# Kernel tuning notes

Measured on AMD Instinct MI355X. Metric: run time of the kernel, lower is better.

Reference implementation:

```python
import jax, jax.numpy as jnp
import numpy as np
import math

IN_DIM = 256
OUT_DIM = 256
H = 4
DK = OUT_DIM // H  # 64
N = 40000
E = 300000
T = 2  # node types
R = 3  # relations: 0:(A->B), 1:(B->A), 2:(A->B)


def setup_inputs() -> dict:
    key = jax.random.key(0)
    ks = jax.random.split(key, 24)
    def xavier(k, shape):
        fan_in, fan_out = shape[-2], shape[-1]
        lim = math.sqrt(6.0 / (fan_in + fan_out))
        return jax.random.uniform(k, shape, jnp.float32, -lim, lim)
    inp = {
        "hA": jax.random.normal(ks[0], (N, IN_DIM), jnp.float32),
        "hB": jax.random.normal(ks[1], (N, IN_DIM), jnp.float32),
        "src0": jax.random.randint(ks[2], (E,), 0, N, jnp.int32),
        "dst0": jax.random.randint(ks[3], (E,), 0, N, jnp.int32),
        "src1": jax.random.randint(ks[4], (E,), 0, N, jnp.int32),
        "dst1": jax.random.randint(ks[5], (E,), 0, N, jnp.int32),
        "src2": jax.random.randint(ks[6], (E,), 0, N, jnp.int32),
        "dst2": jax.random.randint(ks[7], (E,), 0, N, jnp.int32),
        # per-node-type linear weights, stacked [T, in, out]
        "Wk": xavier(ks[8], (T, IN_DIM, OUT_DIM)),
        "bk": jnp.zeros((T, OUT_DIM), jnp.float32),
        "Wq": xavier(ks[9], (T, IN_DIM, OUT_DIM)),
        "bq": jnp.zeros((T, OUT_DIM), jnp.float32),
        "Wv": xavier(ks[10], (T, IN_DIM, OUT_DIM)),
        "bv": jnp.zeros((T, OUT_DIM), jnp.float32),
        "Wa": xavier(ks[11], (T, OUT_DIM, OUT_DIM)),
        "ba": jnp.zeros((T, OUT_DIM), jnp.float32),
        "rel_att": xavier(ks[12], (R, H, DK, DK)),
        "rel_msg": xavier(ks[13], (R, H, DK, DK)),
        "rel_pri": jnp.ones((R, H), jnp.float32),
        "skip": jnp.ones((T,), jnp.float32),
    }
    return inp


def _hgt_forward(hA, hB, Wk, bk, Wq, bq, Wv, bv, Wa, ba,
                 rel_att, rel_msg, rel_pri, skip, edges):
    h = [hA, hB]
    sqrt_dk = math.sqrt(DK)

    def proj(W, b, x, t):
        return (x @ W[t] + b[t]).reshape(-1, H, DK)

    def rel_agg(r, s, d, src, dst):
        # relation-specific transforms
        k = jnp.einsum('nhi,hij->nhj', proj(Wk, bk, h[s], s), rel_att[r])
        v = jnp.einsum('nhi,hij->nhj', proj(Wv, bv, h[s], s), rel_msg[r])
        q = proj(Wq, bq, h[d], d)
        nd = h[d].shape[0]
        # per-edge dot-product attention score [E, H]
        score = jnp.einsum('ehd,ehd->eh', q[dst], k[src]) * rel_pri[r] / sqrt_dk
        # edge softmax normalized by destination node
        m = jax.ops.segment_max(score, dst, num_segments=nd)
        e = jnp.exp(score - m[dst])
        denom = jax.ops.segment_sum(e, dst, num_segments=nd)
        attn = e / denom[dst]
        # weighted scatter-sum aggregation -> [nd, H, DK]
        return jax.ops.segment_sum(v[src] * attn[:, :, None], dst, num_segments=nd)

    (src0, dst0), (src1, dst1), (src2, dst2) = edges
    agg0 = rel_agg(0, 0, 1, src0, dst0)  # A -> B
    agg1 = rel_agg(1, 1, 0, src1, dst1)  # B -> A
    agg2 = rel_agg(2, 0, 1, src2, dst2)  # A -> B

    # cross_reducer='mean' over etypes per destination type
    t_A = agg1.reshape(-1, OUT_DIM)
    t_B = ((agg0 + agg2) * 0.5).reshape(-1, OUT_DIM)

    def ts_aggr(t, n_id, h_dst):
        alpha = jax.nn.sigmoid(skip[n_id])
        trans = t @ Wa[n_id] + ba[n_id]  # dropout p=0.0 -> identity
        return trans * alpha + h_dst * (1.0 - alpha)

    out_A = ts_aggr(t_A, 0, hA)
    out_B = ts_aggr(t_B, 1, hB)
    return jnp.stack([out_A, out_B])  # [2, N, OUT_DIM]


def reference(hA, hB, src0, dst0, src1, dst1, src2, dst2,
              Wk, bk, Wq, bq, Wv, bv, Wa, ba,
              rel_att, rel_msg, rel_pri, skip):
    edges = ((src0, dst0), (src1, dst1), (src2, dst2))
    return _hgt_forward(hA, hB, Wk, bk, Wq, bq, Wv, bv, Wa, ba,
                        rel_att, rel_msg, rel_pri, skip, edges)
```

## Files before the change

kernel.cpp:

```cpp
#include <hip/hip_runtime.h>

#define NN 40000
#define EE 300000
#define DIM 256
#define NHD 4
#define CAP 64
#define LOG2E 1.4426950408889634f

typedef __attribute__((ext_vector_type(8))) short bfrag;
typedef __attribute__((ext_vector_type(4))) float fx4;

static __device__ __forceinline__ float bflo(unsigned u) {
  union { unsigned i; float f; } v; v.i = u << 16; return v.f;
}
static __device__ __forceinline__ float bfhi(unsigned u) {
  union { unsigned i; float f; } v; v.i = u & 0xffff0000u; return v.f;
}
static __device__ __forceinline__ unsigned short f2bf(float f) {
  union { float f; unsigned i; } v; v.f = f;
  unsigned x = v.i;
  return (unsigned short)((x + 0x7fffu + ((x >> 16) & 1u)) >> 16);
}
static __device__ __forceinline__ void gload_lds16(const unsigned short* g, unsigned short* l) {
  __builtin_amdgcn_global_load_lds((const __attribute__((address_space(1))) void*)g,
                                   (__attribute__((address_space(3))) void*)l, 16, 0, 0);
}

static __device__ __forceinline__ void map_rc(int L, int NC, int NR, int& rb, int& cb) {
  int per = 8 * NC;
  int g = L / per;
  int base = g * 8;
  int rig = NR - base; if (rig > 8) rig = 8;
  int idx = L - g * per;
  rb = base + idx % rig;
  cb = idx / rig;
}

static __device__ __forceinline__ void gemm_core64(const unsigned short* __restrict__ X,
                                                   const unsigned short* __restrict__ WT,
                                                   int R0, int C0,
                                                   fx4 acc[2][4],
                                                   unsigned short* ldsA,
                                                   unsigned short* ldsB) {
  const int tid = threadIdx.x;
  const int wave = tid >> 6, lane = tid & 63;
  const int li = lane & 15, lk = lane >> 4;
  const int wr = wave >> 1, wc = wave & 1;
  const int lr = lane >> 3;
  const int swz = ((lane & 7) ^ lr) * 8;
#pragma unroll
  for (int kt = 0; kt < 4; ++kt) {
    const int k0 = kt * 64;
    if (kt) __syncthreads();
#pragma unroll
    for (int i = 0; i < 6; ++i) {
      int g = wave * 6 + i;
      if (g < 8) gload_lds16(X + (size_t)(R0 + g * 8 + lr) * DIM + k0 + swz, ldsA + g * 512);
      else       gload_lds16(WT + (size_t)(C0 + (g - 8) * 8 + lr) * DIM + k0 + swz, ldsB + (g - 8) * 512);
    }
    __syncthreads();
#pragma unroll
    for (int ks = 0; ks < 2; ++ks) {
      bfrag a[2], b[4];
      const int chb = (lk + ks * 4) ^ (li & 7);
#pragma unroll
      for (int mt = 0; mt < 2; ++mt)
        a[mt] = *(const bfrag*)(ldsA + (wr * 32 + mt * 16 + li) * 64 + chb * 8);
#pragma unroll
      for (int nt = 0; nt < 4; ++nt)
        b[nt] = *(const bfrag*)(ldsB + (wc * 64 + nt * 16 + li) * 64 + chb * 8);
#pragma unroll
      for (int mt = 0; mt < 2; ++mt)
#pragma unroll
        for (int nt = 0; nt < 4; ++nt)
          acc[mt][nt] = __builtin_amdgcn_mfma_f32_16x16x32_bf16(a[mt], b[nt], acc[mt][nt], 0, 0, 0);
    }
  }
}

__global__ __launch_bounds__(256) void prep_all(
    const float* __restrict__ hA, const float* __restrict__ hB,
    unsigned short* __restrict__ XA, unsigned short* __restrict__ XB,
    const float* __restrict__ Wk, const float* __restrict__ bk,
    const float* __restrict__ Wq, const float* __restrict__ bq,
    const float* __restrict__ Wv, const float* __restrict__ bv,
    const float* __restrict__ Wa,
    const float* __restrict__ rel_att, const float* __restrict__ rel_msg,
    const float* __restrict__ rel_pri,
    unsigned short* __restrict__ WT_A, unsigned short* __restrict__ WT_B,
    unsigned short* __restrict__ WaT, float* __restrict__ biasA, float* __restrict__ biasB,
    const int* __restrict__ src0, const int* __restrict__ dst0,
    const int* __restrict__ src1, const int* __restrict__ dst1,
    const int* __restrict__ src2, const int* __restrict__ dst2,
    int* __restrict__ cnt, int* __restrict__ bkt) {
  if (blockIdx.x >= 6084) {
    long id = (long)(blockIdx.x - 6084) * 256 + threadIdx.x;
    const long half = (long)NN * DIM / 8;
    const float4* src; unsigned short* dst; long o;
    if (id < half) { src = (const float4*)hA; dst = XA; o = id; }
    else           { src = (const float4*)hB; dst = XB; o = id - half; }
    float4 a = src[o * 2], b = src[o * 2 + 1];
    uint4 pk;
    pk.x = (unsigned)f2bf(a.x) | ((unsigned)f2bf(a.y) << 16);
    pk.y = (unsigned)f2bf(a.z) | ((unsigned)f2bf(a.w) << 16);
    pk.z = (unsigned)f2bf(b.x) | ((unsigned)f2bf(b.y) << 16);
    pk.w = (unsigned)f2bf(b.z) | ((unsigned)f2bf(b.w) << 16);
    ((uint4*)dst)[o] = pk;
    return;
  }
  if (blockIdx.x >= 2568) {
    int bb = blockIdx.x - 2568;
    int r = bb / 1172;
    int e = (bb % 1172) * 256 + threadIdx.x;
    if (e >= EE) return;
    const int* src = r == 0 ? src0 : (r == 1 ? src1 : src2);
    const int* dst = r == 0 ? dst0 : (r == 1 ? dst1 : dst2);
    int d = dst[e];
    int pos = atomicAdd(&cnt[r * NN + d], 1);
    if (pos < CAP) bkt[(size_t)r * NN * CAP + d * CAP + pos] = src[e];
    return;
  }
  int id = blockIdx.x * 256 + threadIdx.x;
  if (id < 262144) {
    int c = id >> 8, i = id & 255;
    int br = c >> 9, w = c & 511, h = w >> 7, ww = w & 127;
    int iskv = (ww >> 2) & 1;
    int j = (ww >> 3) * 4 + (ww & 3);
    int r = br ? 2 : 0;
    const float* W  = iskv ? Wv : Wk;
    const float* RM = iskv ? rel_msg : rel_att;
    const float* wrow = W + i * 256 + h * 64;
    const float* rm = RM + (size_t)((r * NHD + h) * 64) * 64 + j;
    float s = 0.f;
#pragma unroll 8
    for (int l = 0; l < 64; l++) s += wrow[l] * rm[l * 64];
    if (!iskv) s *= rel_pri[r * NHD + h] * 0.125f * LOG2E;
    WT_A[c * 256 + i] = f2bf(s);
    return;
  }
  id -= 262144;
  if (id < 65536) {
    int c = id >> 8, i = id & 255;
    WT_A[(1024 + c) * 256 + i] = f2bf(Wq[i * 256 + c]);
    return;
  }
  id -= 65536;
  if (id < 131072) {
    int c = id >> 8, i = id & 255;
    int h = c >> 7, ww = c & 127;
    int iskv = (ww >> 2) & 1;
    int j = (ww >> 3) * 4 + (ww & 3);
    const float* W  = iskv ? Wv : Wk;
    const float* RM = iskv ? rel_msg : rel_att;
    const float* wrow = W + 65536 + i * 256 + h * 64;
    const float* rm = RM + (size_t)((1 * NHD + h) * 64) * 64 + j;
    float s = 0.f;
#pragma unroll 8
    for (int l = 0; l < 64; l++) s += wrow[l] * rm[l * 64];
    if (!iskv) s *= rel_pri[1 * NHD + h] * 0.125f * LOG2E;
    WT_B[c * 256 + i] = f2bf(s);
    return;
  }
  id -= 131072;
  if (id < 65536) {
    int c = id >> 8, i = id & 255;
    WT_B[(512 + c) * 256 + i] = f2bf(Wq[65536 + i * 256 + c]);
    return;
  }
  id -= 65536;
  if (id < 131072) {
    int t = id >> 16, rem = id & 65535, c = rem >> 8, i = rem & 255;
    WaT[t * 65536 + c * 256 + i] = f2bf(Wa[t * 65536 + i * 256 + c]);
    return;
  }
  id -= 131072;
  if (id < 2048) {
    if (id < 1280) {
      int c = id; float s;
      if (c < 1024) {
        int br = c >> 9, w = c & 511, h = w >> 7, ww = w & 127;
        int iskv = (ww >> 2) & 1;
        int j = (ww >> 3) * 4 + (ww & 3);
        int r = br ? 2 : 0;
        const float* B  = iskv ? bv : bk;
        const float* RM = iskv ? rel_msg : rel_att;
        s = 0.f;
        for (int l = 0; l < 64; l++)
          s += B[h * 64 + l] * RM[(size_t)((r * NHD + h) * 64 + l) * 64 + j];
        if (!iskv) s *= rel_pri[r * NHD + h] * 0.125f * LOG2E;
      } else s = bq[c - 1024];
      biasA[c] = s;
    } else {
      int c = id - 1280; float s;
      if (c < 512) {
        int h = c >> 7, ww = c & 127;
        int iskv = (ww >> 2) & 1;
        int j = (ww >> 3) * 4 + (ww & 3);
        const float* B  = iskv ? bv : bk;
        const float* RM = iskv ? rel_msg : rel_att;
        s = 0.f;
        for (int l = 0; l < 64; l++)
          s += B[256 + h * 64 + l] * RM[(size_t)((1 * NHD + h) * 64 + l) * 64 + j];
        if (!iskv) s *= rel_pri[1 * NHD + h] * 0.125f * LOG2E;
      } else s = bq[256 + (c - 512)];
      biasB[c] = s;
    }
  }
}

__global__ __launch_bounds__(256) void gemm_kvq(const unsigned short* __restrict__ XA,
                                                const unsigned short* __restrict__ XB,
                                                const unsigned short* __restrict__ WT_A,
                                                const unsigned short* __restrict__ WT_B,
                                                const float* __restrict__ biasA,
                                                const float* __restrict__ biasB,
                                                unsigned short* __restrict__ OutA,
                                                unsigned short* __restrict__ OutB) {
  __shared__ unsigned short ldsA[4096], ldsB[8192];
  const unsigned short* X; const unsigned short* WT; const float* bias;
  unsigned short* Out; int ldOut, NC, Lb;
  if (blockIdx.x < 6250) { X = XA; WT = WT_A; bias = biasA; Out = OutA; ldOut = 1280; NC = 10; Lb = blockIdx.x; }
  else                   { X = XB; WT = WT_B; bias = biasB; Out = OutB; ldOut = 768;  NC = 6;  Lb = blockIdx.x - 6250; }
  fx4 acc[2][4] = {};
  int rb, cb; map_rc(Lb, NC, 625, rb, cb);
  const int R0 = rb * 64, C0 = cb * 128;
  gemm_core64(X, WT, R0, C0, acc, ldsA, ldsB);
  const int wave = threadIdx.x >> 6, lane = threadIdx.x & 63;
  const int li = lane & 15, lk = lane >> 4;
  const int wr = wave >> 1, wc = wave & 1;
#pragma unroll
  for (int mt = 0; mt < 2; mt++)
#pragma unroll
    for (int nt = 0; nt < 4; nt++) {
      int col = C0 + wc * 64 + nt * 16 + li;
      float bcol = bias[col];
      int rbase = R0 + wr * 32 + mt * 16 + lk * 4;
#pragma unroll
      for (int i = 0; i < 4; i++)
        Out[(long)(rbase + i) * ldOut + col] = f2bf(acc[mt][nt][i] + bcol);
    }
}

template<int LD>
static __device__ __forceinline__ void proc_bucket(const unsigned short* __restrict__ Out,
                                                   int c, int srcs, int kvoff,
                                                   float q0, float q1, float q2, float q3,
                                                   float& L, float& A0, float& A1, float& A2, float& A3) {
  const uint4 Z = {0u, 0u, 0u, 0u};
  auto ldx = [&](int E) -> uint4 {
    int s = __builtin_amdgcn_readlane(srcs, E & 63);
    return *(const uint4*)(Out + (size_t)s * LD + kvoff);
  };
  auto proc = [&](uint4 u) {
    float pp = q0 * bflo(u.x) + q1 * bfhi(u.x) + q2 * bflo(u.y) + q3 * bfhi(u.y);
    pp += __shfl_xor(pp, 1); pp += __shfl_xor(pp, 2);
    pp += __shfl_xor(pp, 4); pp += __shfl_xor(pp, 8);
    float p = exp2f(pp);
    L += p;
    A0 += p * bflo(u.z); A1 += p * bfhi(u.z);
    A2 += p * bflo(u.w); A3 += p * bfhi(u.w);
  };
  uint4 e0 = Z, e1 = Z, e2 = Z, e3 = Z;
  if (0 < c) e0 = ldx(0);
  if (1 < c) e1 = ldx(1);
  if (2 < c) e2 = ldx(2);
  if (3 < c) e3 = ldx(3);
  for (int e = 0; e < c; e += 4) {
    uint4 f0 = Z, f1 = Z, f2 = Z, f3 = Z;
    if (e + 4 < c) f0 = ldx(e + 4);
    if (e + 5 < c) f1 = ldx(e + 5);
    if (e + 6 < c) f2 = ldx(e + 6);
    if (e + 7 < c) f3 = ldx(e + 7);
    proc(e0);
    if (e + 1 < c) proc(e1);
    if (e + 2 < c) proc(e2);
    if (e + 3 < c) proc(e3);
    e0 = f0; e1 = f1; e2 = f2; e3 = f3;
  }
}

__global__ __launch_bounds__(256) void agg_all(const unsigned short* __restrict__ OutA,
                                               const unsigned short* __restrict__ OutB,
                                               const int* __restrict__ cnt,
                                               const int* __restrict__ bkt,
                                               unsigned short* __restrict__ tA,
                                               unsigned short* __restrict__ tB) {
  int wid = (blockIdx.x * 256 + threadIdx.x) >> 6;
  int lane = threadIdx.x & 63;
  int h = lane >> 4, li = lane & 15;
  int qoff = h * 64 + li * 4;
  int kvoff = h * 128 + li * 8;
  if (wid < NN) {
    int n = wid;
    uint2 qr = *(const uint2*)(OutB + (size_t)n * 768 + 512 + qoff);
    float q0 = bflo(qr.x), q1 = bfhi(qr.x), q2 = bflo(qr.y), q3 = bfhi(qr.y);
    int c0 = min(cnt[n], CAP);
    int c2 = min(cnt[2 * NN + n], CAP);
    int s0 = (lane < c0) ? bkt[(size_t)n * CAP + lane] : 0;
    int s2 = (lane < c2) ? bkt[(size_t)2 * NN * CAP + n * CAP + lane] : 0;
    float l0 = 0.f, b00 = 0.f, b01 = 0.f, b02 = 0.f, b03 = 0.f;
    float l2 = 0.f, b20 = 0.f, b21 = 0.f, b22 = 0.f, b23 = 0.f;
    proc_bucket<1280>(OutA,       c0, s0, kvoff, q0, q1, q2, q3, l0, b00, b01, b02, b03);
    proc_bucket<1280>(OutA + 512, c2, s2, kvoff, q0, q1, q2, q3, l2, b20, b21, b22, b23);
    float i0 = (l0 > 0.f) ? 0.5f / l0 : 0.f;
    float i2 = (l2 > 0.f) ? 0.5f / l2 : 0.f;
    float r0 = b00 * i0 + b20 * i2, r1 = b01 * i0 + b21 * i2;
    float r2 = b02 * i0 + b22 * i2, r3 = b03 * i0 + b23 * i2;
    uint2 pk;
    pk.x = (unsigned)f2bf(r0) | ((unsigned)f2bf(r1) << 16);
    pk.y = (unsigned)f2bf(r2) | ((unsigned)f2bf(r3) << 16);
    *(uint2*)(tB + (size_t)n * DIM + qoff) = pk;
  } else if (wid < 2 * NN) {
    int n = wid - NN;
    uint2 qr = *(const uint2*)(OutA + (size_t)n * 1280 + 1024 + qoff);
    float q0 = bflo(qr.x), q1 = bfhi(qr.x), q2 = bflo(qr.y), q3 = bfhi(qr.y);
    int c = min(cnt[NN + n], CAP);
    int s1 = (lane < c) ? bkt[(size_t)NN * CAP + n * CAP + lane] : 0;
    float l = 0.f, a0 = 0.f, a1 = 0.f, a2 = 0.f, a3 = 0.f;
    proc_bucket<768>(OutB, c, s1, kvoff, q0, q1, q2, q3, l, a0, a1, a2, a3);
    float inv = (l > 0.f) ? 1.f / l : 0.f;
    uint2 pk;
    pk.x = (unsigned)f2bf(a0 * inv) | ((unsigned)f2bf(a1 * inv) << 16);
    pk.y = (unsigned)f2bf(a2 * inv) | ((unsigned)f2bf(a3 * inv) << 16);
    *(uint2*)(tA + (size_t)n * DIM + qoff) = pk;
  }
}

__global__ __launch_bounds__(256) void gemm_final2(const unsigned short* __restrict__ tA,
                                                   const unsigned short* __restrict__ tB,
                                                   const unsigned short* __restrict__ XA,
                                                   const unsigned short* __restrict__ XB,
                                                   const unsigned short* __restrict__ WaT,
                                                   const float* __restrict__ ba,
                                                   const float* __restrict__ skip,
                                                   float* __restrict__ outp) {
  __shared__ unsigned short ldsA[4096], ldsB[8192];
  const int t = blockIdx.y;
  const unsigned short* Tt = t ? tB : tA;
  const unsigned short* hin = t ? XB : XA;
  float* op = outp + (size_t)t * NN * DIM;
  fx4 acc[2][4] = {};
  int rb, cb; map_rc(blockIdx.x, 2, 625, rb, cb);
  const int R0 = rb * 64, C0 = cb * 128;
  gemm_core64(Tt, WaT + t * 65536, R0, C0, acc, ldsA, ldsB);
  const int wave = threadIdx.x >> 6, lane = threadIdx.x & 63;
  const int li = lane & 15, lk = lane >> 4;
  const int wr = wave >> 1, wc = wave & 1;
  float alpha = 1.f / (1.f + __expf(-skip[t]));
  float beta = 1.f - alpha;
#pragma unroll
  for (int mt = 0; mt < 2; mt++)
#pragma unroll
    for (int nt = 0; nt < 4; nt++) {
      int col = C0 + wc * 64 + nt * 16 + li;
      float bcol = ba[t * 256 + col];
      int rbase = R0 + wr * 32 + mt * 16 + lk * 4;
#pragma unroll
      for (int i = 0; i < 4; i++) {
        int row = rbase + i;
        float hv = bflo((unsigned)hin[(size_t)row * DIM + col]);
        op[(long)row * DIM + col] = (acc[mt][nt][i] + bcol) * alpha + hv * beta;
      }
    }
}

extern "C" void kernel_launch(void* const* d_in, const int* in_sizes, int n_in,
                              void* d_out, int out_size, void* d_ws, size_t ws_size,
                              hipStream_t stream) {
  const float* hA = (const float*)d_in[0];
  const float* hB = (const float*)d_in[1];
  const int* src0 = (const int*)d_in[2];
  const int* dst0 = (const int*)d_in[3];
  const int* src1 = (const int*)d_in[4];
  const int* dst1 = (const int*)d_in[5];
  const int* src2 = (const int*)d_in[6];
  const int* dst2 = (const int*)d_in[7];
  const float* Wk = (const float*)d_in[8];
  const float* bk = (const float*)d_in[9];
  const float* Wq = (const float*)d_in[10];
  const float* bq = (const float*)d_in[11];
  const float* Wv = (const float*)d_in[12];
  const float* bv = (const float*)d_in[13];
  const float* Wa = (const float*)d_in[14];
  const float* ba = (const float*)d_in[15];
  const float* rel_att = (const float*)d_in[16];
  const float* rel_msg = (const float*)d_in[17];
  const float* rel_pri = (const float*)d_in[18];
  const float* skip = (const float*)d_in[19];

  char* w = (char*)d_ws;
  unsigned short* XA   = (unsigned short*)(w);
  unsigned short* XB   = (unsigned short*)(w + 20480000);
  unsigned short* OutA = (unsigned short*)(w + 40960000);
  unsigned short* OutB = (unsigned short*)(w + 143360000);
  unsigned short* WT_A = (unsigned short*)(w + 204800000);
  unsigned short* WT_B = (unsigned short*)(w + 205455360);
  unsigned short* WaT  = (unsigned short*)(w + 205848576);
  float* biasA = (float*)(w + 206110720);
  float* biasB = (float*)(w + 206115840);
  int* cnt  = (int*)(w + 206118912);
  int* bkt  = (int*)(w + 206598912);
  unsigned short* tA = (unsigned short*)(w + 237318912);
  unsigned short* tB = (unsigned short*)(w + 257798912);

  hipMemsetAsync(cnt, 0, 3 * NN * sizeof(int), stream);
  prep_all<<<16084, 256, 0, stream>>>(hA, hB, XA, XB,
                                      Wk, bk, Wq, bq, Wv, bv, Wa,
                                      rel_att, rel_msg, rel_pri,
                                      WT_A, WT_B, WaT, biasA, biasB,
                                      src0, dst0, src1, dst1, src2, dst2, cnt, bkt);
  gemm_kvq<<<10000, 256, 0, stream>>>(XA, XB, WT_A, WT_B, biasA, biasB, OutA, OutB);
  agg_all<<<20000, 256, 0, stream>>>(OutA, OutB, cnt, bkt, tA, tB);
  gemm_final2<<<dim3(1250, 2), 256, 0, stream>>>(tA, tB, XA, XB, WaT, ba, skip, (float*)d_out);
}
```

Measured before the change: 353.0 us.

## Fuse edge aggregation with output projection GEMM via LDS-resident tile

Merges the attention aggregation kernel and the final Wa GEMM into one kernel. Each block aggregates 64 destination rows, writes the bf16 results into a swizzled shared-memory tile, and then runs the MFMA GEMM plus the skip blend directly from that tile. This removes the global-memory round trip for the intermediate tA/tB and one kernel launch. In exchange the grid shrinks to 1250 blocks, each wave now processes 16 nodes serially, and each block uses 48KB of LDS, which can lower occupancy and make the latency-bound gather phase slower.

```diff
diff --git a/kernel.cpp b/kernel.cpp
--- a/kernel.cpp
+++ b/kernel.cpp
@@ -279,89 +279,115 @@
   }
 }
 
-__global__ __launch_bounds__(256) void agg_all(const unsigned short* __restrict__ OutA,
-                                               const unsigned short* __restrict__ OutB,
-                                               const int* __restrict__ cnt,
-                                               const int* __restrict__ bkt,
-                                               unsigned short* __restrict__ tA,
-                                               unsigned short* __restrict__ tB) {
-  int wid = (blockIdx.x * 256 + threadIdx.x) >> 6;
-  int lane = threadIdx.x & 63;
-  int h = lane >> 4, li = lane & 15;
-  int qoff = h * 64 + li * 4;
-  int kvoff = h * 128 + li * 8;
-  if (wid < NN) {
-    int n = wid;
-    uint2 qr = *(const uint2*)(OutB + (size_t)n * 768 + 512 + qoff);
-    float q0 = bflo(qr.x), q1 = bfhi(qr.x), q2 = bflo(qr.y), q3 = bfhi(qr.y);
-    int c0 = min(cnt[n], CAP);
-    int c2 = min(cnt[2 * NN + n], CAP);
-    int s0 = (lane < c0) ? bkt[(size_t)n * CAP + lane] : 0;
-    int s2 = (lane < c2) ? bkt[(size_t)2 * NN * CAP + n * CAP + lane] : 0;
-    float l0 = 0.f, b00 = 0.f, b01 = 0.f, b02 = 0.f, b03 = 0.f;
-    float l2 = 0.f, b20 = 0.f, b21 = 0.f, b22 = 0.f, b23 = 0.f;
-    proc_bucket<1280>(OutA,       c0, s0, kvoff, q0, q1, q2, q3, l0, b00, b01, b02, b03);
-    proc_bucket<1280>(OutA + 512, c2, s2, kvoff, q0, q1, q2, q3, l2, b20, b21, b22, b23);
-    float i0 = (l0 > 0.f) ? 0.5f / l0 : 0.f;
-    float i2 = (l2 > 0.f) ? 0.5f / l2 : 0.f;
-    float r0 = b00 * i0 + b20 * i2, r1 = b01 * i0 + b21 * i2;
-    float r2 = b02 * i0 + b22 * i2, r3 = b03 * i0 + b23 * i2;
+__global__ __launch_bounds__(256) void agg_final(const unsigned short* __restrict__ OutA,
+                                                 const unsigned short* __restrict__ OutB,
+                                                 const int* __restrict__ cnt,
+                                                 const int* __restrict__ bkt,
+                                                 const unsigned short* __restrict__ XA,
+                                                 const unsigned short* __restrict__ XB,
+                                                 const unsigned short* __restrict__ WaT,
+                                                 const float* __restrict__ ba,
+                                                 const float* __restrict__ skip,
+                                                 float* __restrict__ outp) {
+  __shared__ unsigned short tT[16384];
+  __shared__ unsigned short ldsB[8192];
+  const int t = blockIdx.y;
+  const int R0 = blockIdx.x * 64;
+  const int wave = threadIdx.x >> 6, lane = threadIdx.x & 63;
+  const int h = lane >> 4, li = lane & 15;
+  const int qoff = h * 64 + li * 4;
+  const int kvoff = h * 128 + li * 8;
+  for (int d = 0; d < 16; ++d) {
+    int row = wave * 16 + d;
+    int n = R0 + row;
+    float r0, r1, r2, r3;
+    if (t) {
+      uint2 qr = *(const uint2*)(OutB + (size_t)n * 768 + 512 + qoff);
+      float q0 = bflo(qr.x), q1 = bfhi(qr.x), q2 = bflo(qr.y), q3 = bfhi(qr.y);
+      int c0 = min(cnt[n], CAP);
+      int c2 = min(cnt[2 * NN + n], CAP);
+      int s0 = (lane < c0) ? bkt[(size_t)n * CAP + lane] : 0;
+      int s2 = (lane < c2) ? bkt[(size_t)2 * NN * CAP + n * CAP + lane] : 0;
+      float l0 = 0.f, b00 = 0.f, b01 = 0.f, b02 = 0.f, b03 = 0.f;
+      float l2 = 0.f, b20 = 0.f, b21 = 0.f, b22 = 0.f, b23 = 0.f;
+      proc_bucket<1280>(OutA,       c0, s0, kvoff, q0, q1, q2, q3, l0, b00, b01, b02, b03);
+      proc_bucket<1280>(OutA + 512, c2, s2, kvoff, q0, q1, q2, q3, l2, b20, b21, b22, b23);
+      float i0 = (l0 > 0.f) ? 0.5f / l0 : 0.f;
+      float i2 = (l2 > 0.f) ? 0.5f / l2 : 0.f;
+      r0 = b00 * i0 + b20 * i2; r1 = b01 * i0 + b21 * i2;
+      r2 = b02 * i0 + b22 * i2; r3 = b03 * i0 + b23 * i2;
+    } else {
+      uint2 qr = *(const uint2*)(OutA + (size_t)n * 1280 + 1024 + qoff);
+      float q0 = bflo(qr.x), q1 = bfhi(qr.x), q2 = bflo(qr.y), q3 = bfhi(qr.y);
+      int c = min(cnt[NN + n], CAP);
+      int s1 = (lane < c) ? bkt[(size_t)NN * CAP + n * CAP + lane] : 0;
+      float l = 0.f, a0 = 0.f, a1 = 0.f, a2 = 0.f, a3 = 0.f;
+      proc_bucket<768>(OutB, c, s1, kvoff, q0, q1, q2, q3, l, a0, a1, a2, a3);
+      float inv = (l > 0.f) ? 1.f / l : 0.f;
+      r0 = a0 * inv; r1 = a1 * inv; r2 = a2 * inv; r3 = a3 * inv;
+    }
     uint2 pk;
     pk.x = (unsigned)f2bf(r0) | ((unsigned)f2bf(r1) << 16);
     pk.y = (unsigned)f2bf(r2) | ((unsigned)f2bf(r3) << 16);
-    *(uint2*)(tB + (size_t)n * DIM + qoff) = pk;
-  } else if (wid < 2 * NN) {
-    int n = wid - NN;
-    uint2 qr = *(const uint2*)(OutA + (size_t)n * 1280 + 1024 + qoff);
-    float q0 = bflo(qr.x), q1 = bfhi(qr.x), q2 = bflo(qr.y), q3 = bfhi(qr.y);
-    int c = min(cnt[NN + n], CAP);
-    int s1 = (lane < c) ? bkt[(size_t)NN * CAP + n * CAP + lane] : 0;
-    float l = 0.f, a0 = 0.f, a1 = 0.f, a2 = 0.f, a3 = 0.f;
-    proc_bucket<768>(OutB, c, s1, kvoff, q0, q1, q2, q3, l, a0, a1, a2, a3);
-    float inv = (l > 0.f) ? 1.f / l : 0.f;
-    uint2 pk;
-    pk.x = (unsigned)f2bf(a0 * inv) | ((unsigned)f2bf(a1 * inv) << 16);
-    pk.y = (unsigned)f2bf(a2 * inv) | ((unsigned)f2bf(a3 * inv) << 16);
-    *(uint2*)(tA + (size_t)n * DIM + qoff) = pk;
-  }
-}
-
-__global__ __launch_bounds__(256) void gemm_final2(const unsigned short* __restrict__ tA,
-                                                   const unsigned short* __restrict__ tB,
-                                                   const unsigned short* __restrict__ XA,
-                                                   const unsigned short* __restrict__ XB,
-                                                   const unsigned short* __restrict__ WaT,
-                                                   const float* __restrict__ ba,
-                                                   const float* __restrict__ skip,
-                                                   float* __restrict__ outp) {
-  __shared__ unsigned short ldsA[4096], ldsB[8192];
-  const int t = blockIdx.y;
-  const unsigned short* Tt = t ? tB : tA;
+    int slot = h * 8 + ((li >> 1) ^ (row & 7));
+    *(uint2*)(tT + row * 256 + slot * 8 + (lane & 1) * 4) = pk;
+  }
+  const int lk = h, wr = wave >> 1, wc = wave & 1;
+  const int lr = lane >> 3;
+  const int swz = ((lane & 7) ^ lr) * 8;
   const unsigned short* hin = t ? XB : XA;
   float* op = outp + (size_t)t * NN * DIM;
-  fx4 acc[2][4] = {};
-  int rb, cb; map_rc(blockIdx.x, 2, 625, rb, cb);
-  const int R0 = rb * 64, C0 = cb * 128;
-  gemm_core64(Tt, WaT + t * 65536, R0, C0, acc, ldsA, ldsB);
-  const int wave = threadIdx.x >> 6, lane = threadIdx.x & 63;
-  const int li = lane & 15, lk = lane >> 4;
-  const int wr = wave >> 1, wc = wave & 1;
   float alpha = 1.f / (1.f + __expf(-skip[t]));
   float beta = 1.f - alpha;
 #pragma unroll
-  for (int mt = 0; mt < 2; mt++)
-#pragma unroll
-    for (int nt = 0; nt < 4; nt++) {
-      int col = C0 + wc * 64 + nt * 16 + li;
-      float bcol = ba[t * 256 + col];
-      int rbase = R0 + wr * 32 + mt * 16 + lk * 4;
-#pragma unroll
-      for (int i = 0; i < 4; i++) {
-        int row = rbase + i;
-        float hv = bflo((unsigned)hin[(size_t)row * DIM + col]);
-        op[(long)row * DIM + col] = (acc[mt][nt][i] + bcol) * alpha + hv * beta;
+  for (int cb = 0; cb < 2; ++cb) {
+    fx4 acc[2][4] = {};
+    const int C0 = cb * 128;
+#pragma unroll
+    for (int kt = 0; kt < 4; ++kt) {
+      __syncthreads();
+#pragma unroll
+      for (int i = 0; i < 4; ++i) {
+        int g = wave * 4 + i;
+        gload_lds16(WaT + (size_t)t * 65536 + (size_t)(C0 + g * 8 + lr) * DIM + kt * 64 + swz,
+                    ldsB + g * 512);
       }
-    }
+      __syncthreads();
+#pragma unroll
+      for (int ks = 0; ks < 2; ++ks) {
+        const int c = lk + ks * 4;
+        bfrag a[2], b[4];
+#pragma unroll
+        for (int mt = 0; mt < 2; ++mt) {
+          int row = wr * 32 + mt * 16 + li;
+          int slot = kt * 8 + (c ^ (li & 7));
+          a[mt] = *(const bfrag*)(tT + row * 256 + slot * 8);
+        }
+#pragma unroll
+        for (int nt = 0; nt < 4; ++nt)
+          b[nt] = *(const bfrag*)(ldsB + (wc * 64 + nt * 16 + li) * 64 + (c ^ (li & 7)) * 8);
+#pragma unroll
+        for (int mt = 0; mt < 2; ++mt)
+#pragma unroll
+          for (int nt = 0; nt < 4; ++nt)
+            acc[mt][nt] = __builtin_amdgcn_mfma_f32_16x16x32_bf16(a[mt], b[nt], acc[mt][nt], 0, 0, 0);
+      }
+    }
+#pragma unroll
+    for (int mt = 0; mt < 2; mt++)
+#pragma unroll
+      for (int nt = 0; nt < 4; nt++) {
+        int col = C0 + wc * 64 + nt * 16 + li;
+        float bcol = ba[t * 256 + col];
+        int rbase = R0 + wr * 32 + mt * 16 + lk * 4;
+#pragma unroll
+        for (int i = 0; i < 4; i++) {
+          int row = rbase + i;
+          float hv = bflo((unsigned)hin[(size_t)row * DIM + col]);
+          op[(long)row * DIM + col] = (acc[mt][nt][i] + bcol) * alpha + hv * beta;
+        }
+      }
+  }
 }
 
 extern "C" void kernel_launch(void* const* d_in, const int* in_sizes, int n_in,
@@ -400,8 +426,6 @@
   float* biasB = (float*)(w + 206115840);
   int* cnt  = (int*)(w + 206118912);
   int* bkt  = (int*)(w + 206598912);
-  unsigned short* tA = (unsigned short*)(w + 237318912);
-  unsigned short* tB = (unsigned short*)(w + 257798912);
 
   hipMemsetAsync(cnt, 0, 3 * NN * sizeof(int), stream);
   prep_all<<<16084, 256, 0, stream>>>(hA, hB, XA, XB,
@@ -410,6 +434,6 @@
                                       WT_A, WT_B, WaT, biasA, biasB,
                                       src0, dst0, src1, dst1, src2, dst2, cnt, bkt);
   gemm_kvq<<<10000, 256, 0, stream>>>(XA, XB, WT_A, WT_B, biasA, biasB, OutA, OutB);
-  agg_all<<<20000, 256, 0, stream>>>(OutA, OutB, cnt, bkt, tA, tB);
-  gemm_final2<<<dim3(1250, 2), 256, 0, stream>>>(tA, tB, XA, XB, WaT, ba, skip, (float*)d_out);
-}
+  agg_final<<<dim3(625, 2), 256, 0, stream>>>(OutA, OutB, cnt, bkt, XA, XB,
+                                              WaT, ba, skip, (float*)d_out);
+}
```

New measurement: 376.1 us. 1.07x slower.
